# Kernel optimization log

Hardware: AMD Instinct MI355X
Metric: run time of the kernel (lower is better)

Reference implementation:

```python
import jax, jax.numpy as jnp
import numpy as np

B, L, D = 32, 2048, 64
MASK_FILL = -1.0e6  # matches torch code's -1000000.0


def setup_inputs() -> dict:
    key = jax.random.key(0)
    kq, kk, kv, kl = jax.random.split(key, 4)
    queries = jax.random.normal(kq, (B, L, D), dtype=jnp.float32)
    keys = jax.random.normal(kk, (B, L, D), dtype=jnp.float32)
    values = jax.random.normal(kv, (B, L, D), dtype=jnp.float32)
    valid_lens = jax.random.randint(kl, (B,), 1, L + 1, dtype=jnp.int64)
    return {"queries": queries, "keys": keys, "values": values,
            "valid_lens": valid_lens}


def reference(queries, keys, values, valid_lens):
    d = queries.shape[-1]
    # [B, Lq, Lk] scores
    scores = jnp.einsum('bqd,bkd->bqk', queries, keys) / jnp.sqrt(
        jnp.asarray(d, dtype=queries.dtype))
    # length mask: position k valid iff k < valid_lens[b]
    Lk = scores.shape[-1]
    mask = jnp.arange(Lk)[None, :] < valid_lens[:, None]      # [B, Lk]
    scores = jnp.where(mask[:, None, :], scores, MASK_FILL)   # broadcast over Lq
    attn = jax.nn.softmax(scores, axis=-1)
    # dropout p=0.0 -> identity
    return jnp.einsum('bqk,bkv->bqv', attn, values)
```

## Files before the change

### kernel.cpp

```cpp
#include <hip/hip_runtime.h>
#include <hip/hip_bf16.h>
#include <math.h>


#define BB 32
#define LL 2048
#define DD 64
#define QBLK 64
#define KBLK 64
#define NTILES (BB * (LL / QBLK))
#define GRID 768

typedef __attribute__((ext_vector_type(8))) short bf16x8;
typedef __attribute__((ext_vector_type(4))) short bf16x4;
typedef __attribute__((ext_vector_type(4))) float f32x4;

static __device__ __forceinline__ short f2bf(float f) {
    __hip_bfloat16 h = __float2bfloat16(f);
    return *reinterpret_cast<short*>(&h);
}
static __device__ __forceinline__ unsigned pk2(float a, float b) {
    return (unsigned)(unsigned short)f2bf(a) | ((unsigned)(unsigned short)f2bf(b) << 16);
}
static __device__ __forceinline__ float exp2c(float x) {
    return __builtin_amdgcn_exp2f(x);
}

static __device__ __forceinline__ f32x4 mfma16(bf16x4 a, bf16x4 b, f32x4 c) {
#if __has_builtin(__builtin_amdgcn_mfma_f32_16x16x16bf16_1k)
    return __builtin_amdgcn_mfma_f32_16x16x16bf16_1k(a, b, c, 0, 0, 0);
#else
    asm("v_mfma_f32_16x16x16_bf16 %0, %1, %2, %0" : "+v"(c) : "v"(a), "v"(b));
    return c;
#endif
}

static __device__ __forceinline__ void cp16(const char* g, char* lbase, int lane) {
#if __has_builtin(__builtin_amdgcn_global_load_lds)
    __builtin_amdgcn_global_load_lds(
        (__attribute__((address_space(1))) void*)g,
        (__attribute__((address_space(3))) void*)lbase, 16, 0, 0);
#else
    *reinterpret_cast<uint4*>(lbase + lane * 16) = *reinterpret_cast<const uint4*>(g);
#endif
}

__global__ void init_ctr_kernel(const int* __restrict__ vlen, int* __restrict__ ws) {
    int t = threadIdx.x;
    if (t == 0) ws[0] = 0;
    if (t < BB) {
        int v = vlen[t];
        int rank = 0;
        for (int j = 0; j < BB; ++j) {
            int vj = vlen[j];
            rank += (vj > v) || (vj == v && j < t);
        }
        ws[1 + rank] = t;
    }
}

__global__ __launch_bounds__(256) void convert_kv_kernel(
    const float* __restrict__ K, const float* __restrict__ V,
    unsigned short* __restrict__ kv)
{
    const int tile = blockIdx.x;
    const int tid  = threadIdx.x;
    const float*  Kt  = K + (size_t)tile * (KBLK * DD);
    const float4* Vg4 = reinterpret_cast<const float4*>(V + (size_t)tile * (KBLK * DD));
    unsigned short* img = kv + (size_t)tile * 8192;

    #pragma unroll
    for (int g = 0; g < 2; ++g) {
        int e = tid + g * 256;
        int f = e >> 6, L = e & 63;
        int t = f >> 1, ds = f & 1;
        int lq = L & 15, lg = L >> 4;
        const float4* src = reinterpret_cast<const float4*>(
            Kt + (t * 16 + lq) * DD + ds * 32 + lg * 8);
        float4 a = src[0], c = src[1];
        uint4 w;
        w.x = pk2(a.x, a.y); w.y = pk2(a.z, a.w);
        w.z = pk2(c.x, c.y); w.w = pk2(c.z, c.w);
        *reinterpret_cast<uint4*>(img + (size_t)e * 8) = w;
    }

    unsigned short* img2 = img + 4096;
    const int vd4 = (tid & 15) * 4;
    const int vkr = (tid >> 4) * 4;
    const int vt  = vkr >> 4;
    const int vlg = (vkr >> 2) & 3;
    float4 v0 = Vg4[(vkr + 0) * 16 + (tid & 15)];
    float4 v1 = Vg4[(vkr + 1) * 16 + (tid & 15)];
    float4 v2 = Vg4[(vkr + 2) * 16 + (tid & 15)];
    float4 v3 = Vg4[(vkr + 3) * 16 + (tid & 15)];
    const float* p0 = (const float*)&v0;
    const float* p1 = (const float*)&v1;
    const float* p2 = (const float*)&v2;
    const float* p3 = (const float*)&v3;
    #pragma unroll
    for (int j = 0; j < 4; ++j) {
        int col = vd4 + j;
        int n = col >> 4, lq = col & 15;
        int L = vlg * 16 + lq;
        uint2 w = make_uint2(pk2(p0[j], p1[j]), pk2(p2[j], p3[j]));
        *reinterpret_cast<uint2*>(img2 + (size_t)(n * 4 + vt) * 256 + L * 4) = w;
    }
}

__global__ __launch_bounds__(256, 2) void attn_mfma_kernel(
    const float* __restrict__ Q, const int* __restrict__ vlen,
    const unsigned short* __restrict__ kvimg,
    float* __restrict__ O, int* __restrict__ ws)
{
    __shared__ __align__(16) unsigned short Buf[3][8192];
    __shared__ int s_tile;

    int* ctr = ws;
    const int* order = ws + 1;

    const int tid  = threadIdx.x;
    const int wid  = tid >> 6;
    const int lane = tid & 63;
    const int lq   = lane & 15;
    const int lg   = lane >> 4;

    const float QSCALE = 0.125f * 1.44269504088896341f;

    for (;;) {
        __syncthreads();
        if (tid == 0) s_tile = atomicAdd(ctr, 1);
        __syncthreads();
        const int tile = s_tile;
        if (tile >= NTILES) break;

        const int b     = order[tile >> 5];
        const int qt    = tile & 31;
        const int qbase = qt * QBLK + wid * 16;
        const int valid = vlen[b];
        const int ntiles = (valid + KBLK - 1) / KBLK;

        const unsigned short* tbase = kvimg + (size_t)b * (32 * 8192);

        auto dma = [&](int t, int bi) {
            const char* g = (const char*)(tbase + (size_t)t * 8192)
                            + wid * 4096 + lane * 16;
            char* l = (char*)&Buf[bi][0] + wid * 4096;
            cp16(g,        l,        lane);
            cp16(g + 1024, l + 1024, lane);
            cp16(g + 2048, l + 2048, lane);
            cp16(g + 3072, l + 3072, lane);
        };

        bf16x8 qf[2];
        {
            const float* Qr = Q + ((size_t)b * LL + qbase + lq) * DD;
            #pragma unroll
            for (int ds_ = 0; ds_ < 2; ++ds_) {
                const float4* p4 = reinterpret_cast<const float4*>(Qr + ds_ * 32 + lg * 8);
                float4 a = p4[0], c = p4[1];
                bf16x8 f;
                f[0] = f2bf(a.x * QSCALE); f[1] = f2bf(a.y * QSCALE);
                f[2] = f2bf(a.z * QSCALE); f[3] = f2bf(a.w * QSCALE);
                f[4] = f2bf(c.x * QSCALE); f[5] = f2bf(c.y * QSCALE);
                f[6] = f2bf(c.z * QSCALE); f[7] = f2bf(c.w * QSCALE);
                qf[ds_] = f;
            }
        }

        f32x4 acc[4];
        #pragma unroll
        for (int n = 0; n < 4; ++n) acc[n] = (f32x4){0.f, 0.f, 0.f, 0.f};
        float m_ = -1e30f, l_ = 0.f;

        auto qkt = [&](int bi, f32x4* s) {
            const unsigned short* kb = &Buf[bi][0];
            __builtin_amdgcn_s_setprio(1);
            #pragma unroll
            for (int t = 0; t < 4; ++t) {
                f32x4 a = (f32x4){0.f, 0.f, 0.f, 0.f};
                #pragma unroll
                for (int ds_ = 0; ds_ < 2; ++ds_) {
                    bf16x8 kf = *reinterpret_cast<const bf16x8*>(
                        &kb[(size_t)(t * 2 + ds_) * 512 + lane * 8]);
                    a = __builtin_amdgcn_mfma_f32_16x16x32_bf16(kf, qf[ds_], a, 0, 0, 0);
                }
                s[t] = a;
            }
            __builtin_amdgcn_s_setprio(0);
        };

        auto smpv = [&](int kt, f32x4* s, int bi) {
            const bool tail = (kt == ntiles - 1) && (valid & (KBLK - 1));
            if (tail) {
                #pragma unroll
                for (int t = 0; t < 4; ++t)
                    #pragma unroll
                    for (int r = 0; r < 4; ++r) {
                        int kg = kt * KBLK + t * 16 + lg * 4 + r;
                        if (kg >= valid) s[t][r] = -1e30f;
                    }
            }
            float mx = s[0][0];
            #pragma unroll
            for (int t = 0; t < 4; ++t)
                #pragma unroll
                for (int r = 0; r < 4; ++r) mx = fmaxf(mx, s[t][r]);
            mx = fmaxf(mx, __shfl_xor(mx, 16, 64));
            mx = fmaxf(mx, __shfl_xor(mx, 32, 64));

            if (__any(mx - m_ > 8.0f)) {
                float mnew = fmaxf(m_, mx);
                float corr = exp2c(m_ - mnew);
                m_ = mnew;
                l_ *= corr;
                #pragma unroll
                for (int r = 0; r < 4; ++r) {
                    float cq = __shfl(corr, lg * 4 + r, 64);
                    #pragma unroll
                    for (int n = 0; n < 4; ++n) acc[n][r] *= cq;
                }
            }

            float ls = 0.f;
            #pragma unroll
            for (int t = 0; t < 4; ++t)
                #pragma unroll
                for (int r = 0; r < 4; ++r) {
                    float p = exp2c(s[t][r] - m_);
                    s[t][r] = p;
                    ls += p;
                }
            ls += __shfl_xor(ls, 16, 64);
            ls += __shfl_xor(ls, 32, 64);
            l_ += ls;

            const unsigned short* vb = &Buf[bi][4096];
            __builtin_amdgcn_s_setprio(1);
            #pragma unroll
            for (int t = 0; t < 4; ++t) {
                union { uint2 u; bf16x4 v; } pa;
                pa.u = make_uint2(pk2(s[t][0], s[t][1]), pk2(s[t][2], s[t][3]));
                #pragma unroll
                for (int n = 0; n < 4; ++n) {
                    union { uint2 u; bf16x4 v; } vv;
                    vv.u = *reinterpret_cast<const uint2*>(
                        &vb[(size_t)(n * 4 + t) * 256 + lane * 4]);
                    acc[n] = mfma16(pa.v, vv.v, acc[n]);
                }
            }
            __builtin_amdgcn_s_setprio(0);
        };

        int bc = 0, bn = 1, bd = 2;
        dma(0, 0);
        if (ntiles > 1) dma(1, 1);
        __syncthreads();
        f32x4 sA[4], sB[4];
        qkt(0, sA);

        int t = 0;
        for (; t + 2 <= ntiles; t += 2) {
            if (t + 2 < ntiles) dma(t + 2, bd);
            qkt(bn, sB);
            smpv(t, sA, bc);
            __syncthreads();
            { int x = bc; bc = bn; bn = bd; bd = x; }
            if (t + 3 < ntiles) dma(t + 3, bd);
            if (t + 2 < ntiles) qkt(bn, sA);
            smpv(t + 1, sB, bc);
            __syncthreads();
            { int x = bc; bc = bn; bn = bd; bd = x; }
        }
        if (t < ntiles) smpv(t, sA, bc);

        float linv[4];
        #pragma unroll
        for (int r = 0; r < 4; ++r)
            linv[r] = 1.f / __shfl(l_, lg * 4 + r, 64);
        float* Ob = O + ((size_t)b * LL + qbase) * DD;
        #pragma unroll
        for (int n = 0; n < 4; ++n) {
            #pragma unroll
            for (int r = 0; r < 4; ++r) {
                Ob[(size_t)(lg * 4 + r) * DD + n * 16 + lq] = acc[n][r] * linv[r];
            }
        }
    }
}

extern "C" void kernel_launch(void* const* d_in, const int* in_sizes, int n_in,
                              void* d_out, int out_size, void* d_ws, size_t ws_size,
                              hipStream_t stream) {
    const float* Q = (const float*)d_in[0];
    const float* K = (const float*)d_in[1];
    const float* V = (const float*)d_in[2];
    const int* vlen = (const int*)d_in[3];
    float* O = (float*)d_out;

    int* ws_i = (int*)d_ws;
    unsigned short* kvimg = (unsigned short*)((char*)d_ws + 1024);

    init_ctr_kernel<<<1, 64, 0, stream>>>(vlen, ws_i);
    convert_kv_kernel<<<BB * (LL / KBLK), 256, 0, stream>>>(K, V, kvimg);
    attn_mfma_kernel<<<GRID, 256, 0, stream>>>(Q, vlen, kvimg, O, ws_i);
}
```

Baseline: 74.41 us.

## Drop LDS staging, read KV image directly per wave with per-wave work tickets

Removes the shared-memory triple-buffered DMA pipeline and block-level barriers. Each wave now takes its own 16-row query ticket via an atomic and loads K/V fragments straight from global memory (relying on L2/cache reuse across waves). The init kernel is folded into the convert kernel to save a launch, and occupancy is raised to 3 blocks per CU. The trade-off is more global/L2 traffic and no explicit prefetch overlap, in exchange for fewer syncs and finer load balancing.

```diff
diff --git a/kernel.cpp b/kernel.cpp
--- a/kernel.cpp
+++ b/kernel.cpp
@@ -6,9 +6,8 @@
 #define BB 32
 #define LL 2048
 #define DD 64
-#define QBLK 64
 #define KBLK 64
-#define NTILES (BB * (LL / QBLK))
+#define NTICKETS 4096
 #define GRID 768
 
 typedef __attribute__((ext_vector_type(8))) short bf16x8;
@@ -25,7 +24,6 @@
 static __device__ __forceinline__ float exp2c(float x) {
     return __builtin_amdgcn_exp2f(x);
 }
-
 static __device__ __forceinline__ f32x4 mfma16(bf16x4 a, bf16x4 b, f32x4 c) {
 #if __has_builtin(__builtin_amdgcn_mfma_f32_16x16x16bf16_1k)
     return __builtin_amdgcn_mfma_f32_16x16x16bf16_1k(a, b, c, 0, 0, 0);
@@ -35,36 +33,27 @@
 #endif
 }
 
-static __device__ __forceinline__ void cp16(const char* g, char* lbase, int lane) {
-#if __has_builtin(__builtin_amdgcn_global_load_lds)
-    __builtin_amdgcn_global_load_lds(
-        (__attribute__((address_space(1))) void*)g,
-        (__attribute__((address_space(3))) void*)lbase, 16, 0, 0);
-#else
-    *reinterpret_cast<uint4*>(lbase + lane * 16) = *reinterpret_cast<const uint4*>(g);
-#endif
-}
-
-__global__ void init_ctr_kernel(const int* __restrict__ vlen, int* __restrict__ ws) {
-    int t = threadIdx.x;
-    if (t == 0) ws[0] = 0;
-    if (t < BB) {
-        int v = vlen[t];
-        int rank = 0;
-        for (int j = 0; j < BB; ++j) {
-            int vj = vlen[j];
-            rank += (vj > v) || (vj == v && j < t);
-        }
-        ws[1 + rank] = t;
-    }
-}
-
 __global__ __launch_bounds__(256) void convert_kv_kernel(
     const float* __restrict__ K, const float* __restrict__ V,
-    unsigned short* __restrict__ kv)
+    const int* __restrict__ vlen, unsigned short* __restrict__ kv,
+    int* __restrict__ ws)
 {
     const int tile = blockIdx.x;
     const int tid  = threadIdx.x;
+
+    if (tile == 0) {
+        if (tid == 32) ws[0] = 0;
+        if (tid < BB) {
+            int v = vlen[tid];
+            int rank = 0;
+            for (int j = 0; j < BB; ++j) {
+                int vj = vlen[j];
+                rank += (vj > v) || (vj == v && j < tid);
+            }
+            ws[1 + rank] = tid;
+        }
+    }
+
     const float*  Kt  = K + (size_t)tile * (KBLK * DD);
     const float4* Vg4 = reinterpret_cast<const float4*>(V + (size_t)tile * (KBLK * DD));
     unsigned short* img = kv + (size_t)tile * 8192;
@@ -107,49 +96,32 @@
     }
 }
 
-__global__ __launch_bounds__(256, 2) void attn_mfma_kernel(
+__global__ __launch_bounds__(256, 3) void attn_mfma_kernel(
     const float* __restrict__ Q, const int* __restrict__ vlen,
     const unsigned short* __restrict__ kvimg,
     float* __restrict__ O, int* __restrict__ ws)
 {
-    __shared__ __align__(16) unsigned short Buf[3][8192];
-    __shared__ int s_tile;
-
     int* ctr = ws;
     const int* order = ws + 1;
 
-    const int tid  = threadIdx.x;
-    const int wid  = tid >> 6;
-    const int lane = tid & 63;
+    const int lane = threadIdx.x & 63;
     const int lq   = lane & 15;
     const int lg   = lane >> 4;
 
     const float QSCALE = 0.125f * 1.44269504088896341f;
 
     for (;;) {
-        __syncthreads();
-        if (tid == 0) s_tile = atomicAdd(ctr, 1);
-        __syncthreads();
-        const int tile = s_tile;
-        if (tile >= NTILES) break;
-
-        const int b     = order[tile >> 5];
-        const int qt    = tile & 31;
-        const int qbase = qt * QBLK + wid * 16;
+        int tk = 0;
+        if (lane == 0) tk = atomicAdd(ctr, 1);
+        tk = __shfl(tk, 0, 64);
+        if (tk >= NTICKETS) break;
+
+        const int b     = order[tk >> 7];
+        const int qbase = (tk & 127) * 16;
         const int valid = vlen[b];
         const int ntiles = (valid + KBLK - 1) / KBLK;
 
         const unsigned short* tbase = kvimg + (size_t)b * (32 * 8192);
-
-        auto dma = [&](int t, int bi) {
-            const char* g = (const char*)(tbase + (size_t)t * 8192)
-                            + wid * 4096 + lane * 16;
-            char* l = (char*)&Buf[bi][0] + wid * 4096;
-            cp16(g,        l,        lane);
-            cp16(g + 1024, l + 1024, lane);
-            cp16(g + 2048, l + 2048, lane);
-            cp16(g + 3072, l + 3072, lane);
-        };
 
         bf16x8 qf[2];
         {
@@ -172,24 +144,30 @@
         for (int n = 0; n < 4; ++n) acc[n] = (f32x4){0.f, 0.f, 0.f, 0.f};
         float m_ = -1e30f, l_ = 0.f;
 
-        auto qkt = [&](int bi, f32x4* s) {
-            const unsigned short* kb = &Buf[bi][0];
-            __builtin_amdgcn_s_setprio(1);
+        for (int kt = 0; kt < ntiles; ++kt) {
+            const unsigned short* ti = tbase + (size_t)kt * 8192;
+
+            f32x4 s[4];
             #pragma unroll
             for (int t = 0; t < 4; ++t) {
                 f32x4 a = (f32x4){0.f, 0.f, 0.f, 0.f};
                 #pragma unroll
                 for (int ds_ = 0; ds_ < 2; ++ds_) {
                     bf16x8 kf = *reinterpret_cast<const bf16x8*>(
-                        &kb[(size_t)(t * 2 + ds_) * 512 + lane * 8]);
+                        &ti[(size_t)(t * 2 + ds_) * 512 + lane * 8]);
                     a = __builtin_amdgcn_mfma_f32_16x16x32_bf16(kf, qf[ds_], a, 0, 0, 0);
                 }
                 s[t] = a;
             }
-            __builtin_amdgcn_s_setprio(0);
-        };
-
-        auto smpv = [&](int kt, f32x4* s, int bi) {
+
+            union { uint2 u; bf16x4 v; } vf[4][4];
+            #pragma unroll
+            for (int t = 0; t < 4; ++t)
+                #pragma unroll
+                for (int n = 0; n < 4; ++n)
+                    vf[t][n].u = *reinterpret_cast<const uint2*>(
+                        &ti[4096 + (size_t)(n * 4 + t) * 256 + lane * 4]);
+
             const bool tail = (kt == ntiles - 1) && (valid & (KBLK - 1));
             if (tail) {
                 #pragma unroll
@@ -234,44 +212,15 @@
             ls += __shfl_xor(ls, 32, 64);
             l_ += ls;
 
-            const unsigned short* vb = &Buf[bi][4096];
-            __builtin_amdgcn_s_setprio(1);
             #pragma unroll
             for (int t = 0; t < 4; ++t) {
                 union { uint2 u; bf16x4 v; } pa;
                 pa.u = make_uint2(pk2(s[t][0], s[t][1]), pk2(s[t][2], s[t][3]));
                 #pragma unroll
-                for (int n = 0; n < 4; ++n) {
-                    union { uint2 u; bf16x4 v; } vv;
-                    vv.u = *reinterpret_cast<const uint2*>(
-                        &vb[(size_t)(n * 4 + t) * 256 + lane * 4]);
-                    acc[n] = mfma16(pa.v, vv.v, acc[n]);
-                }
-            }
-            __builtin_amdgcn_s_setprio(0);
-        };
-
-        int bc = 0, bn = 1, bd = 2;
-        dma(0, 0);
-        if (ntiles > 1) dma(1, 1);
-        __syncthreads();
-        f32x4 sA[4], sB[4];
-        qkt(0, sA);
-
-        int t = 0;
-        for (; t + 2 <= ntiles; t += 2) {
-            if (t + 2 < ntiles) dma(t + 2, bd);
-            qkt(bn, sB);
-            smpv(t, sA, bc);
-            __syncthreads();
-            { int x = bc; bc = bn; bn = bd; bd = x; }
-            if (t + 3 < ntiles) dma(t + 3, bd);
-            if (t + 2 < ntiles) qkt(bn, sA);
-            smpv(t + 1, sB, bc);
-            __syncthreads();
-            { int x = bc; bc = bn; bn = bd; bd = x; }
-        }
-        if (t < ntiles) smpv(t, sA, bc);
+                for (int n = 0; n < 4; ++n)
+                    acc[n] = mfma16(pa.v, vf[t][n].v, acc[n]);
+            }
+        }
 
         float linv[4];
         #pragma unroll
@@ -300,7 +249,6 @@
     int* ws_i = (int*)d_ws;
     unsigned short* kvimg = (unsigned short*)((char*)d_ws + 1024);
 
-    init_ctr_kernel<<<1, 64, 0, stream>>>(vlen, ws_i);
-    convert_kv_kernel<<<BB * (LL / KBLK), 256, 0, stream>>>(K, V, kvimg);
+    convert_kv_kernel<<<BB * (LL / KBLK), 256, 0, stream>>>(K, V, vlen, kvimg, ws_i);
     attn_mfma_kernel<<<GRID, 256, 0, stream>>>(Q, vlen, kvimg, O, ws_i);
 }
```

Result: slower. 184.4 us (+147.8%).
